# Optimization experiments

Measured on AMD Instinct MI355X. Metric: run time of the kernel, lower is better.

The kernel has to match this reference:

```python
import jax, jax.numpy as jnp
import numpy as np

B, N, K, DIM, NB, RES, PAD = 2, 8192, 16, 64, 5, 64, 0.1
H = DIM // 2  # bottleneck width of FKABlock
PLANES = ((0, 1), (0, 2), (1, 2))  # xy, xz, yz


def setup_inputs() -> dict:
    key = jax.random.key(0)
    ks = jax.random.split(key, 10)
    xyz = jax.random.uniform(ks[0], (B, N, 3), jnp.float32) - 0.5

    def w(k, shape, fan_in):
        return jax.random.normal(k, shape, jnp.float32) / np.sqrt(fan_in)

    return {
        "xyz": xyz,
        "w_stem": w(ks[1], (3, DIM), 3),
        "b_stem": jnp.zeros((DIM,), jnp.float32),
        "w0": w(ks[2], (NB, DIM, H), DIM),
        "b0": jnp.zeros((NB, H), jnp.float32),
        "fc1": w(ks[3], (NB, 3, K), 3),
        "fc2": w(ks[4], (NB, 2 * K, K), 2 * K),
        "fc3": w(ks[5], (NB, 2 * K, K), 2 * K),
        "wcv": w(ks[6], (NB, H, H, K), H * K),
        "alpha": jnp.ones((NB,), jnp.float32),
        "beta": jnp.ones((NB,), jnp.float32),
        "w2": w(ks[7], (NB, H, DIM), H),
        "b2": jnp.zeros((NB, DIM), jnp.float32),
    }


def _knn_idx(xyz, k):
    # brute-force squared distances (b, n, n); top-k smallest -> neighbor indices
    sq = jnp.sum(xyz * xyz, -1)
    d2 = sq[:, :, None] + sq[:, None, :] - 2.0 * jnp.einsum('bnd,bmd->bnm', xyz, xyz)
    _, idx = jax.lax.top_k(-d2, k)
    return idx  # (b, n, k) int32


_gather = jax.vmap(lambda f, i: f[i])  # (n, c), (n, k) -> (n, k, c), vmapped over batch


def _fkaconv(x, xyz, idx, fc1, fc2, fc3, wcv, alpha, beta):
    nb_pos = _gather(xyz, idx)                 # (b, n, k, 3)
    pts = nb_pos - xyz[:, :, None, :]          # local coordinates
    # distances are detached in the original (pts.detach())
    dists = jnp.sqrt(jnp.sum(jax.lax.stop_gradient(pts) ** 2, -1) + 1e-12)  # (b, n, k)
    dw = jax.nn.sigmoid(-alpha * dists + beta)
    dw = dw / (jnp.sum(dw, -1, keepdims=True) + 1e-6) * K
    dwe = dw[..., None]                        # (b, n, k, 1)
    # kernel-weight estimation MLP with masked max-pool over neighbors
    m = jax.nn.relu(pts @ fc1)                 # (b, n, k, K)
    mp = jnp.max(m * dwe, 2, keepdims=True)
    m = jax.nn.relu(jnp.concatenate([m, jnp.broadcast_to(mp, m.shape)], -1) @ fc2)
    mp = jnp.max(m * dwe, 2, keepdims=True)
    m = jax.nn.relu(jnp.concatenate([m, jnp.broadcast_to(mp, m.shape)], -1) @ fc3)
    m = m * dwe                                # (b, n, k, K)
    nb_x = _gather(x, idx)                     # (b, n, k, h)
    # f[b,n,c,s] = sum_k nb_x * m ; out[b,n,o] = sum_{c,s} f * wcv[o,c,s]
    return jnp.einsum('bnkc,bnks,ocs->bno', nb_x, m, wcv)


def _triplane(c, xyz):
    pn = xyz / (1.0 + PAD + 1e-3) + 0.5        # normalize to [0, 1]
    ij = jnp.clip((pn * RES).astype(jnp.int32), 0, RES - 1)  # (b, n, 3)
    bidx = jnp.arange(B, dtype=jnp.int32)[:, None]
    cf = c.reshape(B * N, DIM)
    ones = jnp.ones((B * N,), c.dtype)
    planes = []
    for a, b2 in PLANES:
        seg = (bidx * (RES * RES) + ij[..., a] * RES + ij[..., b2]).reshape(-1)
        s = jax.ops.segment_sum(cf, seg, num_segments=B * RES * RES)
        cnt = jax.ops.segment_sum(ones, seg, num_segments=B * RES * RES)
        planes.append((s / jnp.maximum(cnt, 1.0)[:, None]).reshape(B, RES, RES, DIM))
    return jnp.stack(planes, 1)                # (b, 3, res, res, dim)


def reference(xyz, w_stem, b_stem, w0, b0, fc1, fc2, fc3, wcv, alpha, beta, w2, b2):
    c = xyz @ w_stem + b_stem                  # stem linear
    idx = _knn_idx(xyz, K)                     # knn_points(xyz, xyz, K)
    for i in range(NB):                        # FKABlock residual blocks
        x = jax.nn.relu(c @ w0[i] + b0[i])
        x = jax.nn.relu(_fkaconv(x, xyz, idx, fc1[i], fc2[i], fc3[i], wcv[i], alpha[i], beta[i]))
        x = x @ w2[i] + b2[i]
        c = jax.nn.relu(x + c)
    tri_feat = _triplane(c, xyz)
    return (xyz, c, tri_feat)
```

## Files before the change

kernel.cpp:

```cpp
#include <hip/hip_runtime.h>
#include <math.h>

#define BB 2
#define NN 8192
#define KK 16
#define DIMM 64
#define HH 32
#define NBB 5
#define RESS 64
#define NPTS (BB*NN)
#define PLANE_ELEMS (BB*3*RESS*RESS*DIMM)
#define PLANE_CELLS (BB*3*RESS*RESS)
#define GC 8
#define GCS 0.125f
#define NCELL (GC*GC*GC)

__global__ void zero_kernel(float* __restrict__ p, int n) {
  int t = blockIdx.x * blockDim.x + threadIdx.x;
  if (t < n) p[t] = 0.0f;
}

__global__ void stem_kernel(const float* __restrict__ xyz,
                            const float* __restrict__ w,
                            const float* __restrict__ bias,
                            float* __restrict__ out_xyz,
                            float* __restrict__ c) {
  int tid = blockIdx.x * blockDim.x + threadIdx.x;
  if (tid < NPTS*3) out_xyz[tid] = xyz[tid];
  if (tid < NPTS*DIMM) {
    int p = tid >> 6, d = tid & 63;
    float x = xyz[p*3+0], y = xyz[p*3+1], z = xyz[p*3+2];
    c[tid] = x*w[d] + y*w[64+d] + z*w[128+d] + bias[d];
  }
}

__device__ __forceinline__ unsigned ord32(float f) {
  unsigned u = __float_as_uint(f);
  return u ^ ((unsigned)((int)u >> 31) | 0x80000000u);
}
__device__ __forceinline__ int cell_of(float v) {
  return min(max((int)((v + 0.5f) * 8.0f), 0), 7);
}

__global__ void knn_count_kernel(const float* __restrict__ xyz,
                                 int* __restrict__ cellcnt) {
  int p = blockIdx.x * blockDim.x + threadIdx.x;
  if (p >= NPTS) return;
  int bq = p >> 13;
  float px = xyz[p*3], py = xyz[p*3+1], pz = xyz[p*3+2];
  int cc = (cell_of(px) << 6) | (cell_of(py) << 3) | cell_of(pz);
  atomicAdd(&cellcnt[(bq << 9) | cc], 1);
}

__global__ __launch_bounds__(1024) void knn_scan_kernel(const int* __restrict__ cnt,
                                                        int* __restrict__ cellstart,
                                                        int* __restrict__ cellcur) {
  __shared__ int s[1024];
  int t = threadIdx.x;
  int v = cnt[t];
  s[t] = v;
  __syncthreads();
  for (int off = 1; off < 1024; off <<= 1) {
    int add = (t >= off) ? s[t-off] : 0;
    __syncthreads();
    s[t] += add;
    __syncthreads();
  }
  int inc = s[t];
  cellstart[t+1] = inc;
  if (t == 0) cellstart[0] = 0;
  cellcur[t] = inc - v;
}

__global__ void knn_scatter_kernel(const float* __restrict__ xyz,
                                   int* __restrict__ cellcur,
                                   float4* __restrict__ spts) {
  int p = blockIdx.x * blockDim.x + threadIdx.x;
  if (p >= NPTS) return;
  int bq = p >> 13;
  float px = xyz[p*3], py = xyz[p*3+1], pz = xyz[p*3+2];
  int cc = (cell_of(px) << 6) | (cell_of(py) << 3) | cell_of(pz);
  int pos = atomicAdd(&cellcur[(bq << 9) | cc], 1);
  spts[pos] = make_float4(px, py, pz, __int_as_float(p & (NN-1)));
}

#define INS64(key)                                                             \
  {                                                                            \
    unsigned long long _k = (key);                                             \
    _Pragma("unroll")                                                          \
    for (int jj = 15; jj >= 1; --jj) {                                         \
      unsigned long long up = bd[jj-1];                                        \
      bool shift = _k < up;                                                    \
      bool here  = _k < bd[jj];                                                \
      unsigned long long nv = shift ? up : _k;                                 \
      bd[jj] = here ? nv : bd[jj];                                             \
    }                                                                          \
    bd[0] = (_k < bd[0]) ? _k : bd[0];                                         \
  }
#define DRAIN64()                                                              \
  {                                                                            \
    INS64((0 < fcnt) ? fd[0] : ~0ull);                                         \
    INS64((1 < fcnt) ? fd[1] : ~0ull);                                         \
    INS64((2 < fcnt) ? fd[2] : ~0ull);                                         \
    INS64((3 < fcnt) ? fd[3] : ~0ull);                                         \
    fcnt = 0; hi15 = (unsigned)(bd[15] >> 32);                                 \
  }

__global__ __launch_bounds__(64) void knn_query_kernel(
    const float4* __restrict__ spts, const int* __restrict__ cellstart,
    int* __restrict__ idx) {
  int wave = blockIdx.x;
  int b = wave >> 9;
  int cell = wave & 511;
  int cx = cell >> 6, cy = (cell >> 3) & 7, cz = cell & 7;
  int cb = b << 9;
  int qlo = cellstart[cb + cell], qhi = cellstart[cb + cell + 1];
  int nq = qhi - qlo;
  if (nq <= 0) return;
  int lane = threadIdx.x;
  for (int qb = 0; qb < nq; qb += 64) {
    bool valid = (qb + lane) < nq;
    int qpos = qlo + (valid ? qb + lane : 0);
    float4 qv = spts[qpos];
    float qx = qv.x, qy = qv.y, qz = qv.z;
    float qs = qx*qx + qy*qy + qz*qz;
    unsigned long long bd[16];
#pragma unroll
    for (int j = 0; j < 16; ++j) bd[j] = ~0ull;
    unsigned long long fd[4] = {0,0,0,0};
    int fcnt = 0;
    unsigned hi15 = 0xFFFFFFFFu;
    bool done = !valid;
    for (int r = 1; r <= 8; ++r) {
      int x0 = max(cx-r,0), x1 = min(cx+r,7);
      int y0 = max(cy-r,0), y1 = min(cy+r,7);
      int z0 = max(cz-r,0), z1 = min(cz+r,7);
      for (int xx = x0; xx <= x1; ++xx)
      for (int yy = y0; yy <= y1; ++yy)
      for (int zz = z0; zz <= z1; ++zz) {
        if (r > 1) {
          int pr = r - 1;
          if (xx >= cx-pr && xx <= cx+pr && yy >= cy-pr && yy <= cy+pr &&
              zz >= cz-pr && zz <= cz+pr) continue;
        }
        int c2 = cb + (xx << 6) + (yy << 3) + zz;
        int jlo = cellstart[c2], jhi = cellstart[c2+1];
        for (int j = jlo; j < jhi; ++j) {
          float4 c4 = spts[j];
          float sq = c4.x*c4.x + c4.y*c4.y + c4.z*c4.z;
          float d2 = (qs + sq) - 2.0f*(qx*c4.x + qy*c4.y + qz*c4.z);
          unsigned du = ord32(d2);
          if (valid && du <= hi15) {
            unsigned long long key =
                ((unsigned long long)du << 32) | (unsigned)__float_as_int(c4.w);
            fd[0] = (fcnt==0)?key:fd[0];
            fd[1] = (fcnt==1)?key:fd[1];
            fd[2] = (fcnt==2)?key:fd[2];
            fd[3] = (fcnt==3)?key:fd[3];
            fcnt++;
          }
          if (__any(fcnt >= 4)) { DRAIN64(); }
        }
      }
      if (__any(fcnt > 0)) { DRAIN64(); }
      float thr = (float)r * GCS - 1e-4f;
      unsigned thru = ord32(thr * thr);
      done = done || ((unsigned)(bd[15] >> 32) < thru);
      if (!__any(!done)) break;
    }
    if (valid) {
      int n_self = __float_as_int(qv.w);
      int* op = idx + (((long)b << 13) + n_self) * 16;
#pragma unroll
      for (int j = 0; j < 16; ++j) op[j] = (int)(unsigned)(bd[j] & 0xffffffffu);
    }
  }
}

__global__ void xproj_kernel(const float* __restrict__ c,
                             const float* __restrict__ w0,
                             const float* __restrict__ b0,
                             float* __restrict__ x, int layer) {
  int tid = blockIdx.x * blockDim.x + threadIdx.x;
  if (tid >= NPTS*HH) return;
  int p = tid >> 5, h = tid & 31;
  const float* w = w0 + layer*DIMM*HH;
  const float* cr = c + p*DIMM;
  float acc = b0[layer*HH + h];
#pragma unroll
  for (int d = 0; d < DIMM; ++d) acc += cr[d]*w[d*HH + h];
  x[tid] = fmaxf(acc, 0.0f);
}

#define OFF_W1   0
#define OFF_W2AT 48
#define OFF_W2BT 368
#define OFF_W3AT 688
#define OFF_W3BT 1008
#define OFF_WL   1328
#define OFF_B2   3376
#define OFF_RED  3440
#define OFF_Y    4464
#define OFF_SCR  4592
#define SCR_SZ   1296
#define S_DW 0
#define S_M1 16
#define S_M2 272
#define S_MM 528
#define S_XN 784
#define S_FB 16
#define LDS_TOT (OFF_SCR + 4*SCR_SZ)

__global__ __launch_bounds__(256) void conv_kernel(
    float* __restrict__ c, const float* __restrict__ x,
    const int* __restrict__ idx, const float* __restrict__ xyz,
    const float* __restrict__ fc1, const float* __restrict__ fc2,
    const float* __restrict__ fc3, const float* __restrict__ wcv,
    const float* __restrict__ alpha, const float* __restrict__ beta,
    const float* __restrict__ w2, const float* __restrict__ b2, int layer)
{
  __shared__ __align__(16) float lds[LDS_TOT];
  int t = threadIdx.x;

  const float* fc1l = fc1 + layer*3*KK;
  const float* fc2l = fc2 + layer*2*KK*KK;
  const float* fc3l = fc3 + layer*2*KK*KK;
  const float* wcvl = wcv + layer*HH*HH*KK;
  const float* w2l  = w2  + layer*HH*DIMM;
  const float* b2l  = b2  + layer*DIMM;

  if (t < 48) lds[OFF_W1 + t] = fc1l[t];
  {
    int s = t >> 4, tt = t & 15;
    lds[OFF_W2AT + s*20 + tt] = fc2l[tt*16 + s];
    lds[OFF_W2BT + s*20 + tt] = fc2l[(16+tt)*16 + s];
    lds[OFF_W3AT + s*20 + tt] = fc3l[tt*16 + s];
    lds[OFF_W3BT + s*20 + tt] = fc3l[(16+tt)*16 + s];
  }
#pragma unroll
  for (int r = 0; r < 8; ++r) lds[OFF_WL + t + 256*r] = w2l[t + 256*r];
  if (t < 64) lds[OFF_B2 + t] = b2l[t];
  __syncthreads();

  int wv = t >> 6, lane = t & 63;
  int p = blockIdx.x*4 + wv;
  int b = p >> 13;
  float* scr = lds + OFF_SCR + wv*SCR_SZ;
  int sI = lane & 15;

  float qxx = xyz[p*3+0], qyy = xyz[p*3+1], qzz = xyz[p*3+2];
  float alv = alpha[layer], bev = beta[layer];
  int jidx = 0; float px = 0, py = 0, pz = 0, sv = 0;
  if (lane < 16) {
    jidx = idx[p*16 + lane];
    const float* nb = xyz + ((long)b*NN + jidx)*3;
    px = nb[0]-qxx; py = nb[1]-qyy; pz = nb[2]-qzz;
    float dd = sqrtf(px*px + py*py + pz*pz + 1e-12f);
    sv = 1.0f/(1.0f + expf(alv*dd - bev));
  }
  float ssum = 0.0f;
#pragma unroll
  for (int k = 0; k < 16; ++k) ssum += __shfl(sv, k);
  if (lane < 16) scr[S_DW + lane] = sv / (ssum + 1e-6f) * 16.0f;
#pragma unroll
  for (int r = 0; r < 2; ++r) {
    int tsk = lane + 64*r;
    int k = tsk >> 3, seg = tsk & 7;
    int jk = __shfl(jidx, k);
    float4 v = *(const float4*)(x + ((long)b*NN + jk)*32 + seg*4);
    *(float4*)&scr[S_XN + k*32 + seg*4] = v;
  }
#pragma unroll
  for (int r = 0; r < 4; ++r) {
    int k = (lane >> 4) + 4*r;
    float pxk = __shfl(px, k), pyk = __shfl(py, k), pzk = __shfl(pz, k);
    float v = pxk*lds[OFF_W1+sI] + pyk*lds[OFF_W1+16+sI] + pzk*lds[OFF_W1+32+sI];
    scr[S_M1 + k*16 + sI] = fmaxf(v, 0.0f);
  }
  __syncthreads();

  {
    float mpv = 0.0f;
#pragma unroll
    for (int k = 0; k < 16; ++k) mpv = fmaxf(mpv, scr[S_M1 + k*16 + sI] * scr[S_DW + k]);
    float qv = 0.0f;
#pragma unroll
    for (int tt = 0; tt < 16; ++tt) qv += __shfl(mpv, tt) * lds[OFF_W2BT + sI*20 + tt];
    float4 wa0 = *(float4*)&lds[OFF_W2AT + sI*20 + 0];
    float4 wa1 = *(float4*)&lds[OFF_W2AT + sI*20 + 4];
    float4 wa2 = *(float4*)&lds[OFF_W2AT + sI*20 + 8];
    float4 wa3 = *(float4*)&lds[OFF_W2AT + sI*20 + 12];
#pragma unroll
    for (int r = 0; r < 4; ++r) {
      int k = (lane >> 4) + 4*r;
      float4 m0 = *(float4*)&scr[S_M1 + k*16 + 0];
      float4 m1_ = *(float4*)&scr[S_M1 + k*16 + 4];
      float4 m2_ = *(float4*)&scr[S_M1 + k*16 + 8];
      float4 m3_ = *(float4*)&scr[S_M1 + k*16 + 12];
      float v = qv;
      v += m0.x*wa0.x; v += m0.y*wa0.y; v += m0.z*wa0.z; v += m0.w*wa0.w;
      v += m1_.x*wa1.x; v += m1_.y*wa1.y; v += m1_.z*wa1.z; v += m1_.w*wa1.w;
      v += m2_.x*wa2.x; v += m2_.y*wa2.y; v += m2_.z*wa2.z; v += m2_.w*wa2.w;
      v += m3_.x*wa3.x; v += m3_.y*wa3.y; v += m3_.z*wa3.z; v += m3_.w*wa3.w;
      scr[S_M2 + k*16 + sI] = fmaxf(v, 0.0f);
    }
  }
  __syncthreads();

  {
    float mpv = 0.0f;
#pragma unroll
    for (int k = 0; k < 16; ++k) mpv = fmaxf(mpv, scr[S_M2 + k*16 + sI] * scr[S_DW + k]);
    float qv = 0.0f;
#pragma unroll
    for (int tt = 0; tt < 16; ++tt) qv += __shfl(mpv, tt) * lds[OFF_W3BT + sI*20 + tt];
    float4 wa0 = *(float4*)&lds[OFF_W3AT + sI*20 + 0];
    float4 wa1 = *(float4*)&lds[OFF_W3AT + sI*20 + 4];
    float4 wa2 = *(float4*)&lds[OFF_W3AT + sI*20 + 8];
    float4 wa3 = *(float4*)&lds[OFF_W3AT + sI*20 + 12];
#pragma unroll
    for (int r = 0; r < 4; ++r) {
      int k = (lane >> 4) + 4*r;
      float4 m0 = *(float4*)&scr[S_M2 + k*16 + 0];
      float4 m1_ = *(float4*)&scr[S_M2 + k*16 + 4];
      float4 m2_ = *(float4*)&scr[S_M2 + k*16 + 8];
      float4 m3_ = *(float4*)&scr[S_M2 + k*16 + 12];
      float v = qv;
      v += m0.x*wa0.x; v += m0.y*wa0.y; v += m0.z*wa0.z; v += m0.w*wa0.w;
      v += m1_.x*wa1.x; v += m1_.y*wa1.y; v += m1_.z*wa1.z; v += m1_.w*wa1.w;
      v += m2_.x*wa2.x; v += m2_.y*wa2.y; v += m2_.z*wa2.z; v += m2_.w*wa2.w;
      v += m3_.x*wa3.x; v += m3_.y*wa3.y; v += m3_.z*wa3.z; v += m3_.w*wa3.w;
      scr[S_MM + k*16 + sI] = fmaxf(v, 0.0f) * scr[S_DW + k];
    }
  }
  __syncthreads();

  {
    int q4 = lane >> 4;
    float fr0=0,fr1=0,fr2=0,fr3=0,fr4=0,fr5=0,fr6=0,fr7=0;
#pragma unroll
    for (int k = 0; k < 16; ++k) {
      float mmv = scr[S_MM + k*16 + sI];
      float4 a  = *(float4*)&scr[S_XN + k*32 + q4*8];
      float4 bb = *(float4*)&scr[S_XN + k*32 + q4*8 + 4];
      fr0 += a.x*mmv;  fr1 += a.y*mmv;  fr2 += a.z*mmv;  fr3 += a.w*mmv;
      fr4 += bb.x*mmv; fr5 += bb.y*mmv; fr6 += bb.z*mmv; fr7 += bb.w*mmv;
    }
    scr[S_FB + (q4*8+0)*16 + sI] = fr0;
    scr[S_FB + (q4*8+1)*16 + sI] = fr1;
    scr[S_FB + (q4*8+2)*16 + sI] = fr2;
    scr[S_FB + (q4*8+3)*16 + sI] = fr3;
    scr[S_FB + (q4*8+4)*16 + sI] = fr4;
    scr[S_FB + (q4*8+5)*16 + sI] = fr5;
    scr[S_FB + (q4*8+6)*16 + sI] = fr6;
    scr[S_FB + (q4*8+7)*16 + sI] = fr7;
  }
  __syncthreads();

  {
    int o = t & 31, seg = t >> 5;
    const float4* wrow = (const float4*)(wcvl + o*512 + seg*64);
    float acc0=0, acc1=0, acc2=0, acc3=0;
#pragma unroll
    for (int j = 0; j < 16; ++j) {
      float4 w4 = wrow[j];
      float4 f0 = *(const float4*)&lds[OFF_SCR + 0*SCR_SZ + S_FB + seg*64 + j*4];
      float4 f1 = *(const float4*)&lds[OFF_SCR + 1*SCR_SZ + S_FB + seg*64 + j*4];
      float4 f2 = *(const float4*)&lds[OFF_SCR + 2*SCR_SZ + S_FB + seg*64 + j*4];
      float4 f3 = *(const float4*)&lds[OFF_SCR + 3*SCR_SZ + S_FB + seg*64 + j*4];
      acc0 += w4.x*f0.x; acc0 += w4.y*f0.y; acc0 += w4.z*f0.z; acc0 += w4.w*f0.w;
      acc1 += w4.x*f1.x; acc1 += w4.y*f1.y; acc1 += w4.z*f1.z; acc1 += w4.w*f1.w;
      acc2 += w4.x*f2.x; acc2 += w4.y*f2.y; acc2 += w4.z*f2.z; acc2 += w4.w*f2.w;
      acc3 += w4.x*f3.x; acc3 += w4.y*f3.y; acc3 += w4.z*f3.z; acc3 += w4.w*f3.w;
    }
    lds[OFF_RED + seg*128 + 0*32 + o] = acc0;
    lds[OFF_RED + seg*128 + 1*32 + o] = acc1;
    lds[OFF_RED + seg*128 + 2*32 + o] = acc2;
    lds[OFF_RED + seg*128 + 3*32 + o] = acc3;
  }
  __syncthreads();

  if (t < 128) {
    int pt = t >> 5, o = t & 31;
    float yv = 0.0f;
#pragma unroll
    for (int seg = 0; seg < 8; ++seg) yv += lds[OFF_RED + seg*128 + pt*32 + o];
    lds[OFF_Y + pt*32 + o] = fmaxf(yv, 0.0f);
  }
  __syncthreads();

  {
    int pt = t >> 6, d = t & 63;
    float zv = lds[OFF_B2 + d];
#pragma unroll
    for (int o = 0; o < 32; ++o) zv += lds[OFF_Y + pt*32 + o] * lds[OFF_WL + o*64 + d];
    int gp = blockIdx.x*4 + pt;
    float cv = c[gp*64 + d];
    c[gp*64 + d] = fmaxf(zv + cv, 0.0f);
  }
}

__global__ void triacc_kernel(const float* __restrict__ c,
                              const float* __restrict__ xyz,
                              float* __restrict__ psum,
                              float* __restrict__ pcnt) {
  int tid = blockIdx.x * blockDim.x + threadIdx.x;
  if (tid >= NPTS*DIMM) return;
  int p = tid >> 6, d = tid & 63;
  int b = p >> 13;
  float p0 = xyz[p*3+0] / 1.101f + 0.5f;
  float p1 = xyz[p*3+1] / 1.101f + 0.5f;
  float p2 = xyz[p*3+2] / 1.101f + 0.5f;
  int i0 = min(max((int)(p0*64.0f), 0), 63);
  int i1 = min(max((int)(p1*64.0f), 0), 63);
  int i2 = min(max((int)(p2*64.0f), 0), 63);
  int cb = b*3*RESS*RESS;
  int c0 = cb + 0*RESS*RESS + i0*RESS + i1;
  int c1 = cb + 1*RESS*RESS + i0*RESS + i2;
  int c2 = cb + 2*RESS*RESS + i1*RESS + i2;
  float v = c[tid];
  atomicAdd(&psum[c0*DIMM + d], v);
  atomicAdd(&psum[c1*DIMM + d], v);
  atomicAdd(&psum[c2*DIMM + d], v);
  if (d == 0) {
    atomicAdd(&pcnt[c0], 1.0f);
    atomicAdd(&pcnt[c1], 1.0f);
    atomicAdd(&pcnt[c2], 1.0f);
  }
}

__global__ void trinorm_kernel(const float* __restrict__ psum,
                               const float* __restrict__ pcnt,
                               float* __restrict__ out) {
  int tid = blockIdx.x * blockDim.x + threadIdx.x;
  if (tid >= PLANE_ELEMS) return;
  float cnt = pcnt[tid >> 6];
  out[tid] = psum[tid] / fmaxf(cnt, 1.0f);
}

extern "C" void kernel_launch(void* const* d_in, const int* in_sizes, int n_in,
                              void* d_out, int out_size, void* d_ws, size_t ws_size,
                              hipStream_t stream) {
  const float* xyz   = (const float*)d_in[0];
  const float* wstem = (const float*)d_in[1];
  const float* bstem = (const float*)d_in[2];
  const float* w0    = (const float*)d_in[3];
  const float* b0    = (const float*)d_in[4];
  const float* fc1   = (const float*)d_in[5];
  const float* fc2   = (const float*)d_in[6];
  const float* fc3   = (const float*)d_in[7];
  const float* wcv   = (const float*)d_in[8];
  const float* alpha = (const float*)d_in[9];
  const float* beta  = (const float*)d_in[10];
  const float* w2    = (const float*)d_in[11];
  const float* b2    = (const float*)d_in[12];

  float* out     = (float*)d_out;
  float* out_xyz = out;
  float* c       = out + NPTS*3;
  float* out_tri = c + NPTS*DIMM;

  float* wsf  = (float*)d_ws;
  int*   idx  = (int*)d_ws;
  float* x    = wsf + NPTS*16;
  float* psum = x + NPTS*HH;
  float* pcnt = psum + PLANE_ELEMS;

  int*    cellcnt   = (int*)psum;
  int*    cellstart = (int*)psum + 1024;
  int*    cellcur   = (int*)psum + 2056;
  float4* spts      = (float4*)(psum + 4096);

  stem_kernel<<<(NPTS*DIMM+255)/256, 256, 0, stream>>>(xyz, wstem, bstem, out_xyz, c);
  zero_kernel<<<4, 256, 0, stream>>>((float*)cellcnt, 1024);
  knn_count_kernel<<<(NPTS+255)/256, 256, 0, stream>>>(xyz, cellcnt);
  knn_scan_kernel<<<1, 1024, 0, stream>>>(cellcnt, cellstart, cellcur);
  knn_scatter_kernel<<<(NPTS+255)/256, 256, 0, stream>>>(xyz, cellcur, spts);
  knn_query_kernel<<<1024, 64, 0, stream>>>(spts, cellstart, idx);
  for (int layer = 0; layer < NBB; ++layer) {
    xproj_kernel<<<(NPTS*HH+255)/256, 256, 0, stream>>>(c, w0, b0, x, layer);
    conv_kernel<<<NPTS/4, 256, 0, stream>>>(c, x, idx, xyz, fc1, fc2, fc3, wcv,
                                            alpha, beta, w2, b2, layer);
  }
  int nz = PLANE_ELEMS + PLANE_CELLS;
  zero_kernel<<<(nz+255)/256, 256, 0, stream>>>(psum, nz);
  triacc_kernel<<<(NPTS*DIMM+255)/256, 256, 0, stream>>>(c, xyz, psum, pcnt);
  trinorm_kernel<<<(PLANE_ELEMS+255)/256, 256, 0, stream>>>(psum, pcnt, out_tri);
}
```

Before: 591.2 us.

## Stage 3x3x3 neighborhood in LDS and split kNN candidates across 4 lanes per query

The kNN query kernel now copies the 27-cell neighborhood's points into shared memory once per block, using a prefix-sum over cell lengths. Each query is handled by 4 lanes that each scan a quarter of the candidates. The partial top-16 lists are then merged with xor-shuffle steps that skip duplicates. The old deferred-insert buffer is replaced by direct inserts gated on any lane hitting, which targets the poor occupancy of one-query-per-lane and repeated global loads. The trade-offs are a costly 16x16 merge with duplicate checks, a larger shared-memory footprint, and a fallback path when a cell neighborhood exceeds CAP.

```diff
diff --git a/kernel.cpp b/kernel.cpp
--- a/kernel.cpp
+++ b/kernel.cpp
@@ -14,6 +14,7 @@
 #define GC 8
 #define GCS 0.125f
 #define NCELL (GC*GC*GC)
+#define CAP 2496
 
 __global__ void zero_kernel(float* __restrict__ p, int n) {
   int t = blockIdx.x * blockDim.x + threadIdx.x;
@@ -97,18 +98,44 @@
     }                                                                          \
     bd[0] = (_k < bd[0]) ? _k : bd[0];                                         \
   }
-#define DRAIN64()                                                              \
+
+#define TRYKEY(c4)                                                             \
   {                                                                            \
-    INS64((0 < fcnt) ? fd[0] : ~0ull);                                         \
-    INS64((1 < fcnt) ? fd[1] : ~0ull);                                         \
-    INS64((2 < fcnt) ? fd[2] : ~0ull);                                         \
-    INS64((3 < fcnt) ? fd[3] : ~0ull);                                         \
-    fcnt = 0; hi15 = (unsigned)(bd[15] >> 32);                                 \
+    float sq = (c4).x*(c4).x + (c4).y*(c4).y + (c4).z*(c4).z;                  \
+    float d2 = (qs + sq) - 2.0f*(qx*(c4).x + qy*(c4).y + qz*(c4).z);           \
+    unsigned du = ord32(d2);                                                   \
+    bool hit = valid && du <= hi15;                                            \
+    if (__any(hit)) {                                                          \
+      unsigned long long key = hit ?                                           \
+          (((unsigned long long)du << 32) | (unsigned)__float_as_int((c4).w))  \
+          : ~0ull;                                                             \
+      INS64(key);                                                              \
+      hi15 = (unsigned)(bd[15] >> 32);                                         \
+    }                                                                          \
+  }
+
+#define MERGE_STEP(MASK)                                                       \
+  {                                                                            \
+    unsigned long long tmp[16];                                                \
+    _Pragma("unroll")                                                          \
+    for (int j = 0; j < 16; ++j) tmp[j] = __shfl_xor(bd[j], MASK);             \
+    _Pragma("unroll")                                                          \
+    for (int j = 0; j < 16; ++j) {                                             \
+      unsigned long long _in = tmp[j];                                         \
+      bool dup = false;                                                        \
+      _Pragma("unroll")                                                        \
+      for (int jj = 0; jj < 16; ++jj) dup = dup || (bd[jj] == _in);            \
+      INS64(dup ? ~0ull : _in);                                                \
+    }                                                                          \
+    hi15 = (unsigned)(bd[15] >> 32);                                           \
   }
 
 __global__ __launch_bounds__(64) void knn_query_kernel(
     const float4* __restrict__ spts, const int* __restrict__ cellstart,
     int* __restrict__ idx) {
+  __shared__ __align__(16) float4 s_cand[CAP];
+  __shared__ int s_ofs[28];
+  __shared__ int s_jlo[27];
   int wave = blockIdx.x;
   int b = wave >> 9;
   int cell = wave & 511;
@@ -118,57 +145,96 @@
   int nq = qhi - qlo;
   if (nq <= 0) return;
   int lane = threadIdx.x;
-  for (int qb = 0; qb < nq; qb += 64) {
-    bool valid = (qb + lane) < nq;
-    int qpos = qlo + (valid ? qb + lane : 0);
-    float4 qv = spts[qpos];
+  int q = lane & 15, s = lane >> 4;
+
+  int x0 = max(cx-1,0), x1 = min(cx+1,7);
+  int y0 = max(cy-1,0), y1 = min(cy+1,7);
+  int z0 = max(cz-1,0), z1 = min(cz+1,7);
+  int dy = y1-y0+1, dz = z1-z0+1;
+  int count = (x1-x0+1)*dy*dz;
+  int len = 0, jlo0 = 0;
+  if (lane < count) {
+    int xx = x0 + lane/(dy*dz);
+    int rem = lane % (dy*dz);
+    int yy = y0 + rem/dz, zz = z0 + rem % dz;
+    int cc = cb + (xx<<6) + (yy<<3) + zz;
+    jlo0 = cellstart[cc];
+    len = cellstart[cc+1] - jlo0;
+  }
+  int pre = len;
+#pragma unroll
+  for (int off = 1; off < 64; off <<= 1) {
+    int v = __shfl_up(pre, off);
+    if (lane >= off) pre += v;
+  }
+  if (lane < count) { s_ofs[lane] = pre - len; s_jlo[lane] = jlo0; }
+  if (lane == count-1) s_ofs[count] = pre;
+  __syncthreads();
+  int total = s_ofs[count];
+  int tstag = min(total, CAP);
+
+  for (int w = lane; w < tstag; w += 64) {
+    int lo2 = 0, hi2 = count-1;
+    while (lo2 < hi2) { int mid = (lo2+hi2+1)>>1; if (s_ofs[mid] <= w) lo2 = mid; else hi2 = mid-1; }
+    s_cand[w] = spts[s_jlo[lo2] + (w - s_ofs[lo2])];
+  }
+  __syncthreads();
+
+  const unsigned thru1 = ord32((GCS - 1e-4f)*(GCS - 1e-4f));
+  for (int qg = 0; qg < nq; qg += 16) {
+    bool valid = (qg + q) < nq;
+    float4 qv = spts[qlo + qg + (valid ? q : 0)];
     float qx = qv.x, qy = qv.y, qz = qv.z;
     float qs = qx*qx + qy*qy + qz*qz;
     unsigned long long bd[16];
 #pragma unroll
     for (int j = 0; j < 16; ++j) bd[j] = ~0ull;
-    unsigned long long fd[4] = {0,0,0,0};
-    int fcnt = 0;
     unsigned hi15 = 0xFFFFFFFFu;
-    bool done = !valid;
-    for (int r = 1; r <= 8; ++r) {
-      int x0 = max(cx-r,0), x1 = min(cx+r,7);
-      int y0 = max(cy-r,0), y1 = min(cy+r,7);
-      int z0 = max(cz-r,0), z1 = min(cz+r,7);
-      for (int xx = x0; xx <= x1; ++xx)
-      for (int yy = y0; yy <= y1; ++yy)
-      for (int zz = z0; zz <= z1; ++zz) {
-        if (r > 1) {
-          int pr = r - 1;
-          if (xx >= cx-pr && xx <= cx+pr && yy >= cy-pr && yy <= cy+pr &&
-              zz >= cz-pr && zz <= cz+pr) continue;
-        }
-        int c2 = cb + (xx << 6) + (yy << 3) + zz;
-        int jlo = cellstart[c2], jhi = cellstart[c2+1];
-        for (int j = jlo; j < jhi; ++j) {
-          float4 c4 = spts[j];
-          float sq = c4.x*c4.x + c4.y*c4.y + c4.z*c4.z;
-          float d2 = (qs + sq) - 2.0f*(qx*c4.x + qy*c4.y + qz*c4.z);
-          unsigned du = ord32(d2);
-          if (valid && du <= hi15) {
-            unsigned long long key =
-                ((unsigned long long)du << 32) | (unsigned)__float_as_int(c4.w);
-            fd[0] = (fcnt==0)?key:fd[0];
-            fd[1] = (fcnt==1)?key:fd[1];
-            fd[2] = (fcnt==2)?key:fd[2];
-            fd[3] = (fcnt==3)?key:fd[3];
-            fcnt++;
-          }
-          if (__any(fcnt >= 4)) { DRAIN64(); }
+
+    int chunk = (tstag + 3) >> 2;
+    int jb = s*chunk, je = min(jb+chunk, tstag);
+    for (int j = jb; j < je; ++j) {
+      float4 c4 = s_cand[j];
+      TRYKEY(c4);
+    }
+    if (total > CAP) {
+      for (int i = 0; i < count; ++i) {
+        int ofs_i = s_ofs[i], len_i = s_ofs[i+1]-ofs_i;
+        int stg = min(max(CAP - ofs_i, 0), len_i);
+        int jl = s_jlo[i] + stg, jh = s_jlo[i] + len_i;
+        for (int j2 = jl + s; j2 < jh; j2 += 4) {
+          float4 c4 = spts[j2];
+          TRYKEY(c4);
         }
       }
-      if (__any(fcnt > 0)) { DRAIN64(); }
-      float thr = (float)r * GCS - 1e-4f;
-      unsigned thru = ord32(thr * thr);
-      done = done || ((unsigned)(bd[15] >> 32) < thru);
+    }
+    MERGE_STEP(16);
+    MERGE_STEP(32);
+    bool done = !valid || (hi15 < thru1);
+    for (int r = 2; r <= 8; ++r) {
       if (!__any(!done)) break;
-    }
-    if (valid) {
+      int xs0 = max(cx-r,0), xs1 = min(cx+r,7);
+      int ys0 = max(cy-r,0), ys1 = min(cy+r,7);
+      int zs0 = max(cz-r,0), zs1 = min(cz+r,7);
+      int pr = r-1;
+      for (int xx = xs0; xx <= xs1; ++xx)
+      for (int yy = ys0; yy <= ys1; ++yy)
+      for (int zz = zs0; zz <= zs1; ++zz) {
+        if (xx >= cx-pr && xx <= cx+pr && yy >= cy-pr && yy <= cy+pr &&
+            zz >= cz-pr && zz <= cz+pr) continue;
+        int cc2 = cb + (xx<<6) + (yy<<3) + zz;
+        int jl = cellstart[cc2], jh = cellstart[cc2+1];
+        for (int j2 = jl + s; j2 < jh; j2 += 4) {
+          float4 c4 = spts[j2];
+          TRYKEY(c4);
+        }
+      }
+      MERGE_STEP(16);
+      MERGE_STEP(32);
+      float thr2 = (float)r * GCS - 1e-4f;
+      done = !valid || (hi15 < ord32(thr2*thr2));
+    }
+    if (valid && s == 0) {
       int n_self = __float_as_int(qv.w);
       int* op = idx + (((long)b << 13) + n_self) * 16;
 #pragma unroll
```

New measurement: 586.4 us. About the same (-0.8%).
